# Performance work log

Hardware: AMD Instinct MI355X
Metric: run time of the kernel (lower is better)

Reference implementation:

```python
import jax, jax.numpy as jnp
import numpy as np

B, IN, E, H, V, T = 512, 256, 256, 512, 32000, 32


def setup_inputs() -> dict:
    key = jax.random.key(0)
    ks = jax.random.split(key, 8)
    s = 0.05
    return {
        "x": jax.random.normal(ks[0], (B, IN), jnp.float32),
        "agent_w": jax.random.normal(ks[1], (H, IN), jnp.float32) * s,
        "agent_b": jnp.zeros((H,), jnp.float32),
        "sos": jax.random.normal(ks[2], (E,), jnp.float32) * 0.01,
        "emb": jax.random.normal(ks[3], (V, E), jnp.float32) * s,
        "W_ih": jax.random.normal(ks[4], (3 * H, E), jnp.float32) * s,
        "W_hh": jax.random.normal(ks[5], (3 * H, H), jnp.float32) * s,
        "b_ih": jnp.zeros((3 * H,), jnp.float32),
        "b_hh": jnp.zeros((3 * H,), jnp.float32),
        "W_out": jax.random.normal(ks[6], (V, H), jnp.float32) * s,
        "b_out": jnp.zeros((V,), jnp.float32),
        "W_stop": jax.random.normal(ks[7], (1, H), jnp.float32) * s,
        "b_stop": jnp.zeros((1,), jnp.float32),
    }


def _gru_cell(inp, h, W_ih, W_hh, b_ih, b_hh):
    gi = inp @ W_ih.T + b_ih              # [B, 3H]
    gh = h @ W_hh.T + b_hh                # [B, 3H]
    i_r, i_z, i_n = jnp.split(gi, 3, axis=1)
    h_r, h_z, h_n = jnp.split(gh, 3, axis=1)
    r = jax.nn.sigmoid(i_r + h_r)
    z = jax.nn.sigmoid(i_z + h_z)
    n = jnp.tanh(i_n + r * h_n)
    return (1.0 - z) * n + z * h


def reference(x, agent_w, agent_b, sos, emb, W_ih, W_hh, b_ih, b_hh,
              W_out, b_out, W_stop, b_stop):
    h0 = x @ agent_w.T + agent_b                       # agent(x) -> [B, H]
    inp0 = jnp.broadcast_to(sos, (x.shape[0], sos.shape[0]))
    keys = jax.random.split(jax.random.key(42), T)

    def step(carry, k):
        h, inp = carry
        h = _gru_cell(inp, h, W_ih, W_hh, b_ih, b_hh)  # noise_scale=0 -> no noise
        symb_logits = h @ W_out.T + b_out              # [B, V]
        stop_logit = (h @ W_stop.T + b_stop)[:, 0]     # [B]
        logp = jax.nn.log_softmax(symb_logits, axis=1)
        k1, k2 = jax.random.split(k)
        symb = jax.random.categorical(k1, symb_logits, axis=1)          # [B] int
        p_stop = jax.nn.sigmoid(stop_logit)
        stop = jax.random.bernoulli(k2, p_stop).astype(jnp.float32)     # [B]
        symb_lp = jnp.take_along_axis(logp, symb[:, None], axis=1)[:, 0]
        # Bernoulli: log p = s - softplus(s), log(1-p) = -softplus(s)
        sp = jax.nn.softplus(stop_logit)
        stop_lp = stop * stop_logit - sp
        symb_ent = -jnp.sum(jnp.exp(logp) * logp, axis=1)
        stop_ent = sp - stop_logit * p_stop
        inp_next = emb[symb]
        return (h, inp_next), (symb, stop, symb_lp, stop_lp, symb_ent, stop_ent)

    _, ys = jax.lax.scan(step, (h0, inp0), keys)
    symb_seq, stop_seq, symb_lp, stop_lp, symb_ent, stop_ent = ys
    # [T, B] -> [B, T]
    tr = lambda a: a.T
    return (tr(symb_seq), tr(stop_seq).astype(jnp.int32),
            tr(symb_lp), tr(stop_lp), tr(symb_ent), tr(stop_ent))
```

## Files before the change

kernel.cpp:

```cpp
#include <hip/hip_runtime.h>
#include <hip/hip_bf16.h>
#include <stdint.h>

#define JAX_PARTITIONABLE 1

#define Bz 512
#define INz 256
#define Ez 256
#define Hz 512
#define Vz 32000
#define Tz 32
#define BTz (Bz * Tz)
#define TINYF 1.17549435e-38f

typedef float otype;
__device__ __forceinline__ void store_out(otype* out, int idx, float v) {
  out[idx] = v;
}

__device__ __forceinline__ uint32_t rotl32(uint32_t x, int r) {
  return (x << r) | (x >> (32 - r));
}
__device__ __forceinline__ void threefry2x32(uint32_t k0, uint32_t k1,
                                             uint32_t x0, uint32_t x1,
                                             uint32_t& o0, uint32_t& o1) {
  const uint32_t ks2 = k0 ^ k1 ^ 0x1BD11BDAu;
  x0 += k0; x1 += k1;
#define TF_R4(a, b, c, d)                              \
  x0 += x1; x1 = rotl32(x1, a); x1 ^= x0;              \
  x0 += x1; x1 = rotl32(x1, b); x1 ^= x0;              \
  x0 += x1; x1 = rotl32(x1, c); x1 ^= x0;              \
  x0 += x1; x1 = rotl32(x1, d); x1 ^= x0;
  TF_R4(13, 15, 26, 6)  x0 += k1;  x1 += ks2 + 1u;
  TF_R4(17, 29, 16, 24) x0 += ks2; x1 += k0 + 2u;
  TF_R4(13, 15, 26, 6)  x0 += k0;  x1 += k1 + 3u;
  TF_R4(17, 29, 16, 24) x0 += k1;  x1 += ks2 + 4u;
  TF_R4(13, 15, 26, 6)  x0 += ks2; x1 += k0 + 5u;
#undef TF_R4
  o0 = x0; o1 = x1;
}
__device__ __forceinline__ uint32_t rand_bits32(uint32_t ka, uint32_t kb,
                                                uint32_t idx, uint32_t n) {
#if JAX_PARTITIONABLE
  (void)n;
  uint32_t o0, o1;
  threefry2x32(ka, kb, 0u, idx, o0, o1);
  return o0 ^ o1;
#else
  uint32_t half = n >> 1;
  uint32_t o0, o1;
  if (idx < half) { threefry2x32(ka, kb, idx, idx + half, o0, o1); return o0; }
  threefry2x32(ka, kb, idx - half, idx, o0, o1); return o1;
#endif
}
__device__ __forceinline__ float bits_to_f01(uint32_t bits) {
  return __uint_as_float((bits >> 9) | 0x3f800000u) - 1.0f;
}

__global__ void RnnSenderReinforce_36799279792759_kernel(otype* __restrict__ out,
                                                         int n, float v) {
  int i = blockIdx.x * 256 + threadIdx.x;
  if (i < n) out[i] = v;
}

__global__ void keys_kernel(uint32_t* __restrict__ keys) {
  int t = threadIdx.x;
  if (t >= Tz) return;
  uint32_t ka, kb;
#if JAX_PARTITIONABLE
  threefry2x32(0u, 42u, 0u, (uint32_t)t, ka, kb);
#else
  {
    uint32_t j0 = 2u * t, j1 = 2u * t + 1u;
    uint32_t a0, a1, b0, b1;
    if (j0 < Tz) { threefry2x32(0u, 42u, j0, j0 + Tz, a0, a1); ka = a0; }
    else         { threefry2x32(0u, 42u, j0 - Tz, j0, a0, a1); ka = a1; }
    if (j1 < Tz) { threefry2x32(0u, 42u, j1, j1 + Tz, b0, b1); kb = b0; }
    else         { threefry2x32(0u, 42u, j1 - Tz, j1, b0, b1); kb = b1; }
  }
#endif
  uint32_t o0, o1;
#if JAX_PARTITIONABLE
  threefry2x32(ka, kb, 0u, 0u, o0, o1);
  keys[t * 4 + 0] = o0; keys[t * 4 + 1] = o1;
  threefry2x32(ka, kb, 0u, 1u, o0, o1);
  keys[t * 4 + 2] = o0; keys[t * 4 + 3] = o1;
#else
  uint32_t p0, p1, q0, q1;
  threefry2x32(ka, kb, 0u, 2u, p0, p1);
  threefry2x32(ka, kb, 1u, 3u, q0, q1);
  keys[t * 4 + 0] = p0; keys[t * 4 + 1] = q0;
  keys[t * 4 + 2] = p1; keys[t * 4 + 3] = q1;
#endif
}

#define GBM 64
#define GBN 64
#define GBK 32
#define LDSS 68

__global__ __launch_bounds__(256) void gemm_bt(const float* __restrict__ A,
                                               const float* __restrict__ W,
                                               const float* __restrict__ bias,
                                               float* __restrict__ C,
                                               int M, int N, int K) {
  __shared__ __align__(16) float As[GBK * LDSS];
  __shared__ __align__(16) float Bs[GBK * LDSS];
  const int tid = threadIdx.x;
  const int tx = tid & 15;
  const int ty = tid >> 4;
  const int m0 = blockIdx.y * GBM;
  const int n0 = blockIdx.x * GBN;
  const int lr = tid >> 3;
  const int lc = (tid & 7) << 2;

  float acc[4][4] = {};
  const float* Ap = A + (size_t)(m0 + lr) * K + lc;
  const float* Wp = W + (size_t)(n0 + lr) * K + lc;
  const size_t rstep = (size_t)32 * K;

  for (int k0 = 0; k0 < K; k0 += GBK) {
    float4 a0 = *(const float4*)(Ap + k0);
    float4 a1 = *(const float4*)(Ap + k0 + rstep);
    float4 b0 = *(const float4*)(Wp + k0);
    float4 b1 = *(const float4*)(Wp + k0 + rstep);
    __syncthreads();
    As[(lc + 0) * LDSS + lr] = a0.x;
    As[(lc + 1) * LDSS + lr] = a0.y;
    As[(lc + 2) * LDSS + lr] = a0.z;
    As[(lc + 3) * LDSS + lr] = a0.w;
    As[(lc + 0) * LDSS + lr + 32] = a1.x;
    As[(lc + 1) * LDSS + lr + 32] = a1.y;
    As[(lc + 2) * LDSS + lr + 32] = a1.z;
    As[(lc + 3) * LDSS + lr + 32] = a1.w;
    Bs[(lc + 0) * LDSS + lr] = b0.x;
    Bs[(lc + 1) * LDSS + lr] = b0.y;
    Bs[(lc + 2) * LDSS + lr] = b0.z;
    Bs[(lc + 3) * LDSS + lr] = b0.w;
    Bs[(lc + 0) * LDSS + lr + 32] = b1.x;
    Bs[(lc + 1) * LDSS + lr + 32] = b1.y;
    Bs[(lc + 2) * LDSS + lr + 32] = b1.z;
    Bs[(lc + 3) * LDSS + lr + 32] = b1.w;
    __syncthreads();
#pragma unroll
    for (int kk = 0; kk < GBK; kk++) {
      float4 af = *(const float4*)&As[kk * LDSS + (ty << 2)];
      float4 bf = *(const float4*)&Bs[kk * LDSS + (tx << 2)];
      float ar[4] = {af.x, af.y, af.z, af.w};
      float br[4] = {bf.x, bf.y, bf.z, bf.w};
#pragma unroll
      for (int i = 0; i < 4; i++)
#pragma unroll
        for (int j = 0; j < 4; j++)
          acc[i][j] = fmaf(ar[i], br[j], acc[i][j]);
    }
  }

  const int nc = n0 + (tx << 2);
  float4 bv;
  bv.x = bias[nc + 0]; bv.y = bias[nc + 1]; bv.z = bias[nc + 2]; bv.w = bias[nc + 3];
#pragma unroll
  for (int i = 0; i < 4; i++) {
    int m = m0 + (ty << 2) + i;
    float4 o;
    o.x = acc[i][0] + bv.x;
    o.y = acc[i][1] + bv.y;
    o.z = acc[i][2] + bv.z;
    o.w = acc[i][3] + bv.w;
    *(float4*)(C + (size_t)m * N + nc) = o;
  }
}

#define TBM 128
#define TBN 128
#define TBK 32
#define TLDP 132

__global__ __launch_bounds__(256) void gemm128_bt(const float* __restrict__ A,
                                                  const float* __restrict__ W,
                                                  const float* __restrict__ bias,
                                                  float* __restrict__ C,
                                                  int M, int N, int K) {
  __shared__ __align__(16) float As[TBK * TLDP];
  __shared__ __align__(16) float Bs[TBK * TLDP];
  const int tid = threadIdx.x;
  const int tx = tid & 15;
  const int ty = tid >> 4;
  const int m0 = blockIdx.y * TBM;
  const int n0 = blockIdx.x * TBN;

  const int sr = tid >> 1;
  const int sk = (tid & 1) << 4;

  const float* Ap = A + (size_t)(m0 + sr) * K + sk;
  const float* Wp = W + (size_t)(n0 + sr) * K + sk;

  float4 a[4], b[4];
#pragma unroll
  for (int i = 0; i < 4; i++) {
    a[i] = *(const float4*)(Ap + i * 4);
    b[i] = *(const float4*)(Wp + i * 4);
  }

  float acc[8][8] = {};

  for (int k0 = 0; k0 < K; k0 += TBK) {
    __syncthreads();
#pragma unroll
    for (int i = 0; i < 4; i++) {
      float av[4] = {a[i].x, a[i].y, a[i].z, a[i].w};
      float bw[4] = {b[i].x, b[i].y, b[i].z, b[i].w};
#pragma unroll
      for (int j = 0; j < 4; j++) {
        As[(sk + i * 4 + j) * TLDP + sr] = av[j];
        Bs[(sk + i * 4 + j) * TLDP + sr] = bw[j];
      }
    }
    __syncthreads();
    if (k0 + TBK < K) {
#pragma unroll
      for (int i = 0; i < 4; i++) {
        a[i] = *(const float4*)(Ap + (k0 + TBK) + i * 4);
        b[i] = *(const float4*)(Wp + (k0 + TBK) + i * 4);
      }
    }
#pragma unroll 4
    for (int kk = 0; kk < TBK; kk++) {
      float4 a0 = *(const float4*)&As[kk * TLDP + (ty << 2)];
      float4 a1 = *(const float4*)&As[kk * TLDP + 64 + (ty << 2)];
      float4 b0 = *(const float4*)&Bs[kk * TLDP + (tx << 2)];
      float4 b1 = *(const float4*)&Bs[kk * TLDP + 64 + (tx << 2)];
      float ar[8] = {a0.x, a0.y, a0.z, a0.w, a1.x, a1.y, a1.z, a1.w};
      float br[8] = {b0.x, b0.y, b0.z, b0.w, b1.x, b1.y, b1.z, b1.w};
#pragma unroll
      for (int i = 0; i < 8; i++)
#pragma unroll
        for (int j = 0; j < 8; j++)
          acc[i][j] = fmaf(ar[i], br[j], acc[i][j]);
    }
  }

  const int nc0 = n0 + (tx << 2);
  const float4 bv0 = *(const float4*)(bias + nc0);
  const float4 bv1 = *(const float4*)(bias + nc0 + 64);
#pragma unroll
  for (int hf = 0; hf < 2; hf++) {
#pragma unroll
    for (int i = 0; i < 4; i++) {
      const int m = m0 + hf * 64 + (ty << 2) + i;
      float* Cp = C + (size_t)m * N + nc0;
      float4 o;
      o.x = acc[hf * 4 + i][0] + bv0.x;
      o.y = acc[hf * 4 + i][1] + bv0.y;
      o.z = acc[hf * 4 + i][2] + bv0.z;
      o.w = acc[hf * 4 + i][3] + bv0.w;
      *(float4*)Cp = o;
      float4 o2;
      o2.x = acc[hf * 4 + i][4] + bv1.x;
      o2.y = acc[hf * 4 + i][5] + bv1.y;
      o2.z = acc[hf * 4 + i][6] + bv1.z;
      o2.w = acc[hf * 4 + i][7] + bv1.w;
      *(float4*)(Cp + 64) = o2;
    }
  }
}

__global__ void gates_kernel(const float* __restrict__ gi,
                             const float* __restrict__ gh,
                             float* __restrict__ h) {
  int idx = blockIdx.x * 256 + threadIdx.x;
  int b = idx >> 9;
  int j = idx & 511;
  const float* gib = gi + (size_t)b * (3 * Hz);
  const float* ghb = gh + (size_t)b * (3 * Hz);
  float ir = gib[j], iz = gib[j + Hz], in_ = gib[j + 2 * Hz];
  float hr = ghb[j], hz = ghb[j + Hz], hn = ghb[j + 2 * Hz];
  float r = 1.0f / (1.0f + expf(-(ir + hr)));
  float z = 1.0f / (1.0f + expf(-(iz + hz)));
  float n = tanhf(in_ + r * hn);
  float hv = h[idx];
  h[idx] = (1.0f - z) * n + z * hv;
}

__global__ __launch_bounds__(256) void stop_kernel(const float* __restrict__ h,
                                                   const float* __restrict__ W_stop,
                                                   const float* __restrict__ b_stop,
                                                   const uint32_t* __restrict__ keys,
                                                   int t, otype* __restrict__ out) {
  int wave = threadIdx.x >> 6;
  int lane = threadIdx.x & 63;
  int b = blockIdx.x * 4 + wave;
  const float* hb = h + (size_t)b * Hz;
  float s = 0.0f;
  for (int k = lane; k < Hz; k += 64) s = fmaf(hb[k], W_stop[k], s);
#pragma unroll
  for (int off = 32; off; off >>= 1) s += __shfl_down(s, off, 64);
  if (lane == 0) {
    s += b_stop[0];
    uint32_t bits = rand_bits32(keys[t * 4 + 2], keys[t * 4 + 3], (uint32_t)b, Bz);
    float u = bits_to_f01(bits);
    float p = 1.0f / (1.0f + expf(-s));
    float stop = (u < p) ? 1.0f : 0.0f;
    float sp = fmaxf(s, 0.0f) + log1pf(expf(-fabsf(s)));
    store_out(out, 1 * BTz + b * Tz + t, stop);
    store_out(out, 3 * BTz + b * Tz + t, stop * s - sp);
    store_out(out, 5 * BTz + b * Tz + t, sp - s * p);
  }
}

__global__ __launch_bounds__(256) void sample_kernel(const float* __restrict__ logits,
                                                     const uint32_t* __restrict__ keys,
                                                     int t, otype* __restrict__ out,
                                                     int* __restrict__ symb_i) {
  __shared__ float sm[256], sg[256], sgl[256], sz[256], ss[256];
  __shared__ int sgi[256];
  const int tid = threadIdx.x;
  const int b = blockIdx.x;
  const float* lb = logits + (size_t)b * Vz;
  const uint32_t k1a = keys[t * 4 + 0], k1b = keys[t * 4 + 1];
  const uint32_t base = (uint32_t)b * (uint32_t)Vz;

  float m = -INFINITY, gbest = -INFINITY, glogit = 0.0f;
  int gidx = 0x7FFFFFFF;
  for (int v = tid; v < Vz; v += 256) {
    float l = lb[v];
    m = fmaxf(m, l);
    uint32_t bits = rand_bits32(k1a, k1b, base + (uint32_t)v, (uint32_t)Bz * Vz);
    float f = bits_to_f01(bits);
    float u = fmaxf(TINYF, f + TINYF);
    float g = -logf(-logf(u));
    float val = l + g;
    if (val > gbest) { gbest = val; gidx = v; glogit = l; }
  }
  sm[tid] = m; sg[tid] = gbest; sgi[tid] = gidx; sgl[tid] = glogit;
  __syncthreads();
  for (int s2 = 128; s2; s2 >>= 1) {
    if (tid < s2) {
      sm[tid] = fmaxf(sm[tid], sm[tid + s2]);
      float go = sg[tid + s2]; int io = sgi[tid + s2];
      if (go > sg[tid] || (go == sg[tid] && io < sgi[tid])) {
        sg[tid] = go; sgi[tid] = io; sgl[tid] = sgl[tid + s2];
      }
    }
    __syncthreads();
  }
  const float M = sm[0];

  float Z = 0.0f, S1 = 0.0f;
  for (int v = tid; v < Vz; v += 256) {
    float sft = lb[v] - M;
    float e = expf(sft);
    Z += e;
    S1 = fmaf(e, sft, S1);
  }
  sz[tid] = Z; ss[tid] = S1;
  __syncthreads();
  for (int s2 = 128; s2; s2 >>= 1) {
    if (tid < s2) { sz[tid] += sz[tid + s2]; ss[tid] += ss[tid + s2]; }
    __syncthreads();
  }
  if (tid == 0) {
    float Zt = sz[0], S1t = ss[0];
    float lse = logf(Zt);
    int symb = sgi[0];
    store_out(out, 0 * BTz + b * Tz + t, (float)symb);
    store_out(out, 2 * BTz + b * Tz + t, (sgl[0] - M) - lse);
    store_out(out, 4 * BTz + b * Tz + t, lse - S1t / Zt);
    symb_i[b] = symb;
  }
}

__global__ void init_inp_kernel(float* __restrict__ inp, const float* __restrict__ sos) {
  inp[blockIdx.x * Ez + threadIdx.x] = sos[threadIdx.x];
}
__global__ void gather_kernel(const float* __restrict__ emb,
                              const int* __restrict__ symb_i,
                              float* __restrict__ inp) {
  int b = blockIdx.x;
  int s = symb_i[b];
  s = (s < 0) ? 0 : ((s >= Vz) ? (Vz - 1) : s);
  inp[(size_t)b * Ez + threadIdx.x] = emb[(size_t)s * Ez + threadIdx.x];
}

extern "C" __attribute__((visibility("default")))
void kernel_launch(void* const* d_in, const int* in_sizes, int n_in,
                   void* d_out, int out_size, void* d_ws, size_t ws_size,
                   hipStream_t stream) {
  const float* x       = (const float*)d_in[0];
  const float* agent_w = (const float*)d_in[1];
  const float* agent_b = (const float*)d_in[2];
  const float* sos     = (const float*)d_in[3];
  const float* emb     = (const float*)d_in[4];
  const float* W_ih    = (const float*)d_in[5];
  const float* W_hh    = (const float*)d_in[6];
  const float* b_ih    = (const float*)d_in[7];
  const float* b_hh    = (const float*)d_in[8];
  const float* W_out   = (const float*)d_in[9];
  const float* b_out   = (const float*)d_in[10];
  const float* W_stop  = (const float*)d_in[11];
  const float* b_stop  = (const float*)d_in[12];
  otype* out = (otype*)d_out;

  float* ws = (float*)d_ws;
  float* h      = ws;
  float* inp    = h + (size_t)Bz * Hz;
  float* gi     = inp + (size_t)Bz * Ez;
  float* gh     = gi + (size_t)Bz * 3 * Hz;
  float* logits = gh + (size_t)Bz * 3 * Hz;
  int* symb_i   = (int*)(logits + (size_t)Bz * Vz);
  uint32_t* keys = (uint32_t*)(symb_i + Bz);

  keys_kernel<<<1, 64, 0, stream>>>(keys);
  init_inp_kernel<<<Bz, Ez, 0, stream>>>(inp, sos);
  gemm_bt<<<dim3(Hz / GBN, Bz / GBM), 256, 0, stream>>>(x, agent_w, agent_b, h,
                                                        Bz, Hz, INz);
  for (int t = 0; t < Tz; t++) {
    gemm_bt<<<dim3(3 * Hz / GBN, Bz / GBM), 256, 0, stream>>>(inp, W_ih, b_ih, gi,
                                                              Bz, 3 * Hz, Ez);
    gemm_bt<<<dim3(3 * Hz / GBN, Bz / GBM), 256, 0, stream>>>(h, W_hh, b_hh, gh,
                                                              Bz, 3 * Hz, Hz);
    gates_kernel<<<(Bz * Hz) / 256, 256, 0, stream>>>(gi, gh, h);
    gemm128_bt<<<dim3(Vz / TBN, Bz / TBM), 256, 0, stream>>>(h, W_out, b_out,
                                                             logits, Bz, Vz, Hz);
    stop_kernel<<<Bz / 4, 256, 0, stream>>>(h, W_stop, b_stop, keys, t, out);
    sample_kernel<<<Bz, 256, 0, stream>>>(logits, keys, t, out, symb_i);
    gather_kernel<<<Bz, Ez, 0, stream>>>(emb, symb_i, inp);
  }
}
```

Baseline: 11.54 ms.

## Fuse GRU input/hidden GEMMs and enlarge vocab projection tile with swizzled grid

The two per-step GRU GEMMs (input and hidden) now run in one launch, with blockIdx.z picking which one a block computes. The W_out logits GEMM moves from 128x128 tiles on 256 threads to 256x128 tiles on 512 threads. It also uses a 1D grid that groups blocks so neighbouring blocks share W_out column panels, aiming at better L2 reuse. The larger tile halves the number of times W_out is streamed, but raises LDS use per block and may lower occupancy.

After: 10.82 ms. 1.07x faster.

```diff
diff --git a/kernel.cpp b/kernel.cpp
--- a/kernel.cpp
+++ b/kernel.cpp
@@ -99,18 +99,18 @@
 #define GBK 32
 #define LDSS 68
 
-__global__ __launch_bounds__(256) void gemm_bt(const float* __restrict__ A,
-                                               const float* __restrict__ W,
-                                               const float* __restrict__ bias,
-                                               float* __restrict__ C,
-                                               int M, int N, int K) {
-  __shared__ __align__(16) float As[GBK * LDSS];
-  __shared__ __align__(16) float Bs[GBK * LDSS];
+__device__ __forceinline__ void gemm_bt_body(const float* __restrict__ A,
+                                             const float* __restrict__ W,
+                                             const float* __restrict__ bias,
+                                             float* __restrict__ C,
+                                             int M, int N, int K,
+                                             int bx, int by,
+                                             float* As, float* Bs) {
   const int tid = threadIdx.x;
   const int tx = tid & 15;
   const int ty = tid >> 4;
-  const int m0 = blockIdx.y * GBM;
-  const int n0 = blockIdx.x * GBN;
+  const int m0 = by * GBM;
+  const int n0 = bx * GBN;
   const int lr = tid >> 3;
   const int lc = (tid & 7) << 2;
 
@@ -171,72 +171,131 @@
   }
 }
 
-#define TBM 128
-#define TBN 128
-#define TBK 32
-#define TLDP 132
-
-__global__ __launch_bounds__(256) void gemm128_bt(const float* __restrict__ A,
-                                                  const float* __restrict__ W,
-                                                  const float* __restrict__ bias,
-                                                  float* __restrict__ C,
-                                                  int M, int N, int K) {
-  __shared__ __align__(16) float As[TBK * TLDP];
-  __shared__ __align__(16) float Bs[TBK * TLDP];
+__global__ __launch_bounds__(256) void gemm_bt(const float* __restrict__ A,
+                                               const float* __restrict__ W,
+                                               const float* __restrict__ bias,
+                                               float* __restrict__ C,
+                                               int M, int N, int K) {
+  __shared__ __align__(16) float As[GBK * LDSS];
+  __shared__ __align__(16) float Bs[GBK * LDSS];
+  gemm_bt_body(A, W, bias, C, M, N, K, blockIdx.x, blockIdx.y, As, Bs);
+}
+
+__global__ __launch_bounds__(256) void gru2_kernel(const float* __restrict__ inp,
+                                                   const float* __restrict__ Wih,
+                                                   const float* __restrict__ bih,
+                                                   float* __restrict__ gi,
+                                                   const float* __restrict__ h,
+                                                   const float* __restrict__ Whh,
+                                                   const float* __restrict__ bhh,
+                                                   float* __restrict__ gh) {
+  __shared__ __align__(16) float As[GBK * LDSS];
+  __shared__ __align__(16) float Bs[GBK * LDSS];
+  if (blockIdx.z == 0)
+    gemm_bt_body(inp, Wih, bih, gi, Bz, 3 * Hz, Ez, blockIdx.x, blockIdx.y, As, Bs);
+  else
+    gemm_bt_body(h, Whh, bhh, gh, Bz, 3 * Hz, Hz, blockIdx.x, blockIdx.y, As, Bs);
+}
+
+#define QBM 256
+#define QBN 128
+#define QBK 32
+#define QLDA 260
+#define QLDB 132
+
+__global__ __launch_bounds__(512, 4) void gemm256_bt(const float* __restrict__ A,
+                                                     const float* __restrict__ W,
+                                                     const float* __restrict__ bias,
+                                                     float* __restrict__ C,
+                                                     int M, int N, int K) {
+  __shared__ __align__(16) float As[QBK * QLDA];
+  __shared__ __align__(16) float Bs[QBK * QLDB];
   const int tid = threadIdx.x;
   const int tx = tid & 15;
   const int ty = tid >> 4;
-  const int m0 = blockIdx.y * TBM;
-  const int n0 = blockIdx.x * TBN;
-
-  const int sr = tid >> 1;
-  const int sk = (tid & 1) << 4;
-
-  const float* Ap = A + (size_t)(m0 + sr) * K + sk;
-  const float* Wp = W + (size_t)(n0 + sr) * K + sk;
-
-  float4 a[4], b[4];
-#pragma unroll
-  for (int i = 0; i < 4; i++) {
-    a[i] = *(const float4*)(Ap + i * 4);
-    b[i] = *(const float4*)(Wp + i * 4);
-  }
+
+  const int nP = N / QBN;
+  const int G = nP >> 3;
+  const int lim = G << 4;
+  int b = blockIdx.x;
+  int P, mi;
+  if (b < lim) {
+    int g = b >> 4, r = b & 15;
+    mi = r >> 3;
+    P = (g << 3) + (r & 7);
+  } else {
+    int e = b - lim;
+    P = (G << 3) + (e & 1);
+    mi = e >> 1;
+  }
+  const int m0 = mi * QBM;
+  const int n0 = P * QBN;
+
+  const int ar = tid >> 1;
+  const int ak = (tid & 1) << 4;
+  const int br = tid >> 2;
+  const int bk = (tid & 3) << 2;
+
+  const float* Ap = A + (size_t)(m0 + ar) * K + ak;
+  const float* Wp = W + (size_t)(n0 + br) * K + bk;
+
+  float4 a0 = *(const float4*)(Ap);
+  float4 a1 = *(const float4*)(Ap + 4);
+  float4 a2 = *(const float4*)(Ap + 8);
+  float4 a3 = *(const float4*)(Ap + 12);
+  float4 b0 = *(const float4*)(Wp);
+  float4 b1 = *(const float4*)(Wp + 16);
 
   float acc[8][8] = {};
 
-  for (int k0 = 0; k0 < K; k0 += TBK) {
-    __syncthreads();
-#pragma unroll
-    for (int i = 0; i < 4; i++) {
-      float av[4] = {a[i].x, a[i].y, a[i].z, a[i].w};
-      float bw[4] = {b[i].x, b[i].y, b[i].z, b[i].w};
-#pragma unroll
-      for (int j = 0; j < 4; j++) {
-        As[(sk + i * 4 + j) * TLDP + sr] = av[j];
-        Bs[(sk + i * 4 + j) * TLDP + sr] = bw[j];
-      }
-    }
-    __syncthreads();
-    if (k0 + TBK < K) {
-#pragma unroll
-      for (int i = 0; i < 4; i++) {
-        a[i] = *(const float4*)(Ap + (k0 + TBK) + i * 4);
-        b[i] = *(const float4*)(Wp + (k0 + TBK) + i * 4);
-      }
+  for (int k0 = 0; k0 < K; k0 += QBK) {
+    __syncthreads();
+    As[(ak + 0) * QLDA + ar] = a0.x;
+    As[(ak + 1) * QLDA + ar] = a0.y;
+    As[(ak + 2) * QLDA + ar] = a0.z;
+    As[(ak + 3) * QLDA + ar] = a0.w;
+    As[(ak + 4) * QLDA + ar] = a1.x;
+    As[(ak + 5) * QLDA + ar] = a1.y;
+    As[(ak + 6) * QLDA + ar] = a1.z;
+    As[(ak + 7) * QLDA + ar] = a1.w;
+    As[(ak + 8) * QLDA + ar] = a2.x;
+    As[(ak + 9) * QLDA + ar] = a2.y;
+    As[(ak + 10) * QLDA + ar] = a2.z;
+    As[(ak + 11) * QLDA + ar] = a2.w;
+    As[(ak + 12) * QLDA + ar] = a3.x;
+    As[(ak + 13) * QLDA + ar] = a3.y;
+    As[(ak + 14) * QLDA + ar] = a3.z;
+    As[(ak + 15) * QLDA + ar] = a3.w;
+    Bs[(bk + 0) * QLDB + br] = b0.x;
+    Bs[(bk + 1) * QLDB + br] = b0.y;
+    Bs[(bk + 2) * QLDB + br] = b0.z;
+    Bs[(bk + 3) * QLDB + br] = b0.w;
+    Bs[(16 + bk + 0) * QLDB + br] = b1.x;
+    Bs[(16 + bk + 1) * QLDB + br] = b1.y;
+    Bs[(16 + bk + 2) * QLDB + br] = b1.z;
+    Bs[(16 + bk + 3) * QLDB + br] = b1.w;
+    __syncthreads();
+    if (k0 + QBK < K) {
+      a0 = *(const float4*)(Ap + k0 + QBK);
+      a1 = *(const float4*)(Ap + k0 + QBK + 4);
+      a2 = *(const float4*)(Ap + k0 + QBK + 8);
+      a3 = *(const float4*)(Ap + k0 + QBK + 12);
+      b0 = *(const float4*)(Wp + k0 + QBK);
+      b1 = *(const float4*)(Wp + k0 + QBK + 16);
     }
 #pragma unroll 4
-    for (int kk = 0; kk < TBK; kk++) {
-      float4 a0 = *(const float4*)&As[kk * TLDP + (ty << 2)];
-      float4 a1 = *(const float4*)&As[kk * TLDP + 64 + (ty << 2)];
-      float4 b0 = *(const float4*)&Bs[kk * TLDP + (tx << 2)];
-      float4 b1 = *(const float4*)&Bs[kk * TLDP + 64 + (tx << 2)];
-      float ar[8] = {a0.x, a0.y, a0.z, a0.w, a1.x, a1.y, a1.z, a1.w};
-      float br[8] = {b0.x, b0.y, b0.z, b0.w, b1.x, b1.y, b1.z, b1.w};
+    for (int kk = 0; kk < QBK; kk++) {
+      float4 xa0 = *(const float4*)&As[kk * QLDA + (ty << 2)];
+      float4 xa1 = *(const float4*)&As[kk * QLDA + 128 + (ty << 2)];
+      float4 xb0 = *(const float4*)&Bs[kk * QLDB + (tx << 2)];
+      float4 xb1 = *(const float4*)&Bs[kk * QLDB + 64 + (tx << 2)];
+      float ar8[8] = {xa0.x, xa0.y, xa0.z, xa0.w, xa1.x, xa1.y, xa1.z, xa1.w};
+      float br8[8] = {xb0.x, xb0.y, xb0.z, xb0.w, xb1.x, xb1.y, xb1.z, xb1.w};
 #pragma unroll
       for (int i = 0; i < 8; i++)
 #pragma unroll
         for (int j = 0; j < 8; j++)
-          acc[i][j] = fmaf(ar[i], br[j], acc[i][j]);
+          acc[i][j] = fmaf(ar8[i], br8[j], acc[i][j]);
     }
   }
 
@@ -247,7 +306,7 @@
   for (int hf = 0; hf < 2; hf++) {
 #pragma unroll
     for (int i = 0; i < 4; i++) {
-      const int m = m0 + hf * 64 + (ty << 2) + i;
+      const int m = m0 + hf * 128 + (ty << 2) + i;
       float* Cp = C + (size_t)m * N + nc0;
       float4 o;
       o.x = acc[hf * 4 + i][0] + bv0.x;
@@ -415,13 +474,11 @@
   gemm_bt<<<dim3(Hz / GBN, Bz / GBM), 256, 0, stream>>>(x, agent_w, agent_b, h,
                                                         Bz, Hz, INz);
   for (int t = 0; t < Tz; t++) {
-    gemm_bt<<<dim3(3 * Hz / GBN, Bz / GBM), 256, 0, stream>>>(inp, W_ih, b_ih, gi,
-                                                              Bz, 3 * Hz, Ez);
-    gemm_bt<<<dim3(3 * Hz / GBN, Bz / GBM), 256, 0, stream>>>(h, W_hh, b_hh, gh,
-                                                              Bz, 3 * Hz, Hz);
+    gru2_kernel<<<dim3(3 * Hz / GBN, Bz / GBM, 2), 256, 0, stream>>>(
+        inp, W_ih, b_ih, gi, h, W_hh, b_hh, gh);
     gates_kernel<<<(Bz * Hz) / 256, 256, 0, stream>>>(gi, gh, h);
-    gemm128_bt<<<dim3(Vz / TBN, Bz / TBM), 256, 0, stream>>>(h, W_out, b_out,
-                                                             logits, Bz, Vz, Hz);
+    gemm256_bt<<<(Vz / QBN) * (Bz / QBM), 512, 0, stream>>>(h, W_out, b_out,
+                                                            logits, Bz, Vz, Hz);
     stop_kernel<<<Bz / 4, 256, 0, stream>>>(h, W_stop, b_stop, keys, t, out);
     sample_kernel<<<Bz, 256, 0, stream>>>(logits, keys, t, out, symb_i);
     gather_kernel<<<Bz, Ez, 0, stream>>>(emb, symb_i, inp);
```
